# Kernel optimization log

Measured on AMD Instinct MI355X. Metric: run time of the kernel, lower is better.

Reference implementation:

```python
import jax, jax.numpy as jnp
import numpy as np

NUM_LAYERS = 2
NUM_DIR = 2
HID = 512
INP = 1024  # = NUM_DIR * HID so all layers share weight shapes
R = 8
ALPHA = 16
SCALING = ALPHA / R  # 2.0
BATCH = 32
SEQ = 512


def _lstm_dir(x, w_ih, w_hh, b_ih, b_hh, a_ih, bl_ih, a_hh, bl_hh, reverse):
    """One direction of one layer. x: (B,T,D). Returns (out (B,T,H), h_T, c_T)."""
    Bn = x.shape[0]
    # Input-dependent part of the gates is time-parallel: frozen ih matmul,
    # both biases, and the ih LoRA branch (shared A, per-gate B blocks are
    # just the stacked (4H, r) matrix).
    gx = jnp.einsum('btd,gd->btg', x, w_ih) + b_ih + b_hh
    gx = gx + SCALING * jnp.einsum('btr,gr->btg', jnp.einsum('btd,rd->btr', x, a_ih), bl_ih)
    gx = jnp.swapaxes(gx, 0, 1)  # (T,B,4H)
    h0 = jnp.zeros((Bn, HID), x.dtype)
    c0 = jnp.zeros((Bn, HID), x.dtype)

    def step(carry, g_t):
        h, c = carry
        gates = g_t + h @ w_hh.T + SCALING * ((h @ a_hh.T) @ bl_hh.T)
        i, f, g, o = jnp.split(gates, 4, axis=-1)  # torch gate order i,f,g,o
        c = jax.nn.sigmoid(f) * c + jax.nn.sigmoid(i) * jnp.tanh(g)
        h = jax.nn.sigmoid(o) * jnp.tanh(c)
        return (h, c), h

    (hT, cT), hs = jax.lax.scan(step, (h0, c0), gx, reverse=reverse)
    return jnp.swapaxes(hs, 0, 1), hT, cT


def _forward(x, w_ih, w_hh, b_ih, b_hh, a_ih, bl_ih, a_hh, bl_hh):
    layer_in = x
    h_all, c_all = [], []
    for layer in range(NUM_LAYERS):
        outs = []
        for d in range(NUM_DIR):
            idx = layer * NUM_DIR + d
            o, hT, cT = _lstm_dir(layer_in, w_ih[idx], w_hh[idx], b_ih[idx], b_hh[idx],
                                  a_ih[idx], bl_ih[idx], a_hh[idx], bl_hh[idx],
                                  reverse=(d == 1))
            outs.append(o)
            h_all.append(hT)
            c_all.append(cT)
        layer_in = jnp.concatenate(outs, axis=-1)  # (B,T,2H)
        # inter-layer dropout is 0.0 -> identity
    return layer_in, jnp.stack(h_all), jnp.stack(c_all)


def setup_inputs() -> dict:
    key = jax.random.key(0)
    ks = jax.random.split(key, 10)
    G = 4 * HID
    NC = NUM_LAYERS * NUM_DIR  # 4 cells
    s_ih = 1.0 / np.sqrt(INP)
    s_hh = 1.0 / np.sqrt(HID)
    return {
        'x': jax.random.normal(ks[0], (BATCH, SEQ, INP), jnp.float32),
        'w_ih': jax.random.normal(ks[1], (NC, G, INP), jnp.float32) * s_ih,
        'w_hh': jax.random.normal(ks[2], (NC, G, HID), jnp.float32) * s_hh,
        'b_ih': jax.random.normal(ks[3], (NC, G), jnp.float32) * s_hh,
        'b_hh': jax.random.normal(ks[4], (NC, G), jnp.float32) * s_hh,
        'a_ih': jax.random.normal(ks[5], (NC, R, INP), jnp.float32) * s_ih,
        'bl_ih': jax.random.normal(ks[6], (NC, G, R), jnp.float32) * 0.01,
        'a_hh': jax.random.normal(ks[7], (NC, R, HID), jnp.float32) * s_hh,
        'bl_hh': jax.random.normal(ks[8], (NC, G, R), jnp.float32) * 0.01,
    }


def reference(x, w_ih, w_hh, b_ih, b_hh, a_ih, bl_ih, a_hh, bl_hh):
    out, h_n, c_n = _forward(x, w_ih, w_hh, b_ih, b_hh, a_ih, bl_ih, a_hh, bl_hh)
    return out, h_n, c_n
```

## Files before the change

kernel.cpp:

```cpp
#include <hip/hip_runtime.h>
#include <stdint.h>


typedef unsigned short u16;
typedef unsigned long long u64;
typedef __bf16 bf16x8 __attribute__((ext_vector_type(8)));
typedef float f32x4 __attribute__((ext_vector_type(4)));

#define NCELL 4
#define HID 512
#define INP 1024
#define G4 2048
#define BATCH 32
#define SEQ 512
#define RLORA 8
#define NW 16
#define HPW 32
#define HTAGN 8192

__device__ __forceinline__ float bf2f(u16 u) {
  union { uint32_t i; float f; } v;
  v.i = ((uint32_t)u) << 16;
  return v.f;
}
__device__ __forceinline__ u16 f2bf(float f) {
  union { float f; uint32_t i; } v;
  v.f = f;
  uint32_t lsb = (v.i >> 16) & 1;
  return (u16)((v.i + 0x7fffu + lsb) >> 16);
}
__device__ __forceinline__ float sigm(float x) {
  return __builtin_amdgcn_rcpf(1.f + __expf(-x));
}
__device__ __forceinline__ float ftanh(float x) {
  return 1.f - 2.f * __builtin_amdgcn_rcpf(__expf(2.f * x) + 1.f);
}

template <int K>
__global__ void fold_kernel(const float* __restrict__ w, const float* __restrict__ a,
                            const float* __restrict__ bl, u16* __restrict__ weff) {
  int64_t idx = (int64_t)blockIdx.x * blockDim.x + threadIdx.x;
  if (idx >= (int64_t)NCELL * G4 * K) return;
  int d = (int)(idx % K);
  int64_t gc = idx / K;
  int cell = (int)(gc / G4);
  float acc = w[idx];
#pragma unroll
  for (int r = 0; r < RLORA; ++r)
    acc += 2.0f * bl[gc * RLORA + r] * a[(int64_t)cell * RLORA * K + r * K + d];
  weff[idx] = f2bf(acc);
}

__global__ void bias_kernel(const float* __restrict__ b_ih, const float* __restrict__ b_hh,
                            float* __restrict__ bias) {
  int i = blockIdx.x * blockDim.x + threadIdx.x;
  if (i < NCELL * G4) bias[i] = b_ih[i] + b_hh[i];
}

template <bool AF32>
__global__ __launch_bounds__(256) void gemm_kernel(const void* __restrict__ Ain,
                                                   const u16* __restrict__ W,
                                                   const float* __restrict__ bias,
                                                   u16* __restrict__ gx, int tw0, int tw1,
                                                   int CL) {
  __shared__ alignas(16) u16 As[128][72];
  __shared__ alignas(16) u16 Bs[128][72];
  const int tid = threadIdx.x;
  const int dir = blockIdx.z;
  const int m0 = blockIdx.x * 128;
  const int n0 = blockIdx.y * 128;
  const int tw = dir ? tw1 : tw0;
  const int Mc = BATCH * CL;
  const u16* Wc = W + (int64_t)dir * G4 * INP;
  const float* bc = bias + dir * G4;
  u16* gxc = gx + (int64_t)dir * Mc * G4;
  const int wave = tid >> 6, lane = tid & 63;
  const int wm = wave & 1, wn = wave >> 1;
  const int llo = lane & 15, lhi = lane >> 4;

  int64_t aoff[4];
  const u16* bptr[4];
  int srow[4], ssc[4];
#pragma unroll
  for (int i = 0; i < 4; ++i) {
    int s = i * 256 + tid;
    srow[i] = s >> 3;
    ssc[i] = s & 7;
    int lr = m0 + srow[i];
    int b = lr / CL;
    int tt = tw + (lr - b * CL);
    aoff[i] = ((int64_t)b * SEQ + tt) * INP + ssc[i] * 8;
    bptr[i] = Wc + (int64_t)(n0 + srow[i]) * INP + ssc[i] * 8;
  }

  const f32x4 fzero = {0.f, 0.f, 0.f, 0.f};
  f32x4 acc[4][4];
#pragma unroll
  for (int i = 0; i < 4; ++i)
#pragma unroll
    for (int j = 0; j < 4; ++j) acc[i][j] = fzero;

  for (int kt = 0; kt < INP / 64; ++kt) {
    const int kb = kt * 64;
    __syncthreads();
#pragma unroll
    for (int i = 0; i < 4; ++i) {
      if (AF32) {
        const float* src = (const float*)Ain + aoff[i] + kb;
        uint32_t p[4];
#pragma unroll
        for (int q = 0; q < 4; ++q)
          p[q] = (uint32_t)f2bf(src[2 * q]) | ((uint32_t)f2bf(src[2 * q + 1]) << 16);
        *(uint4*)&As[srow[i]][ssc[i] * 8] = make_uint4(p[0], p[1], p[2], p[3]);
      } else {
        *(uint4*)&As[srow[i]][ssc[i] * 8] = *(const uint4*)((const u16*)Ain + aoff[i] + kb);
      }
      *(uint4*)&Bs[srow[i]][ssc[i] * 8] = *(const uint4*)(bptr[i] + kb);
    }
    __syncthreads();
#pragma unroll
    for (int ks = 0; ks < 2; ++ks) {
      bf16x8 af[4], bfr[4];
#pragma unroll
      for (int i = 0; i < 4; ++i) {
        af[i] = *(const bf16x8*)&As[wm * 64 + i * 16 + llo][ks * 32 + lhi * 8];
        bfr[i] = *(const bf16x8*)&Bs[wn * 64 + i * 16 + llo][ks * 32 + lhi * 8];
      }
#pragma unroll
      for (int i = 0; i < 4; ++i)
#pragma unroll
        for (int j = 0; j < 4; ++j)
          acc[i][j] = __builtin_amdgcn_mfma_f32_16x16x32_bf16(af[i], bfr[j], acc[i][j], 0, 0, 0);
    }
  }
#pragma unroll
  for (int i = 0; i < 4; ++i) {
    const int lr0 = m0 + wm * 64 + i * 16 + lhi * 4;
#pragma unroll
    for (int j = 0; j < 4; ++j) {
      const int ncol = n0 + wn * 64 + j * 16 + llo;
      const float bv = bc[ncol];
#pragma unroll
      for (int r = 0; r < 4; ++r) gxc[(int64_t)(lr0 + r) * G4 + ncol] = f2bf(acc[i][j][r] + bv);
    }
  }
}

template <bool OUTF32>
__global__ __launch_bounds__(256, 1) void rec_kernel(
    const u16* __restrict__ gx,
    const u16* __restrict__ Whh,
    u64* __restrict__ htag,
    void* __restrict__ outp,
    float* __restrict__ hn, float* __restrict__ cn,
    float* __restrict__ cstate,
    int cell_base, int s0, int CL) {
  const int tid = threadIdx.x;
  const int dir = blockIdx.x / NW;
  const int wg = blockIdx.x % NW;
  const int hb = wg * HPW;
  const int wave = tid >> 6, lane = tid & 63;
  const int llo = lane & 15, lhi = lane >> 4;
  const int Mc = BATCH * CL;

  const u16* gxc = gx + (int64_t)dir * Mc * G4;
  const u16* Wc = Whh + (int64_t)dir * G4 * HID;
  u64* ht_dir = htag + (int64_t)dir * (2 * HTAGN);
  float* cst = cstate + (int64_t)(cell_base + dir) * BATCH * HID;

  __shared__ alignas(16) u16 h_lds[2 * 16 * 64 * 8];
  __shared__ float g_lds[4][BATCH][HPW + 1];

  uint4 wfrag[2][16];
#pragma unroll
  for (int j = 0; j < 2; ++j)
#pragma unroll
    for (int ks = 0; ks < 16; ++ks) {
      const int col = wave * HID + hb + j * 16 + llo;
      wfrag[j][ks] = *(const uint4*)(Wc + (int64_t)col * HID + ks * 32 + lhi * 8);
    }
  if (s0 == 0) {
    for (int i = tid; i < 2 * 16 * 64 * 8 / 2; i += 256) ((uint32_t*)h_lds)[i] = 0;
  }
  const int cb = tid >> 3, j0 = (tid & 7) * 4;
  float creg[4];
#pragma unroll
  for (int u = 0; u < 4; ++u) creg[u] = (s0 == 0) ? 0.f : cst[cb * HID + hb + j0 + u];
  const int wmt = cb >> 4, wllo = cb & 15, wlhi = j0 >> 3, wjof = j0 & 7;
  const int64_t wfragidx = ((int64_t)((wmt * 16 + wg) * 64 + wlhi * 16 + wllo) * 8 + wjof) >> 2;
  u64* const wpkt_base = ht_dir + 2 * wfragidx;

  for (int s = s0; s < s0 + CL; ++s) {
    const int ls = s - s0;
    const int t = dir ? (SEQ - 1 - s) : s;
    const int lcol = dir ? (CL - 1 - ls) : ls;
    f32x4 acc[2][2];
#pragma unroll
    for (int mt = 0; mt < 2; ++mt)
#pragma unroll
      for (int j = 0; j < 2; ++j) {
        const int col = wave * HID + hb + j * 16 + llo;
#pragma unroll
        for (int r = 0; r < 4; ++r) {
          const int b = mt * 16 + lhi * 4 + r;
          acc[mt][j][r] = bf2f(gxc[(int64_t)(b * CL + lcol) * G4 + col]);
        }
      }
    if (s > 0) {
      u64* src = ht_dir + ((s - 1) & 1) * HTAGN;
      const uint32_t want = (uint32_t)s;
      u64 va[16], vb[16];
#pragma unroll
      for (int k = 0; k < 16; ++k) {
        const int idx = tid + k * 256;
        va[k] = __hip_atomic_load(src + 2 * idx, __ATOMIC_RELAXED, __HIP_MEMORY_SCOPE_AGENT);
        vb[k] = __hip_atomic_load(src + 2 * idx + 1, __ATOMIC_RELAXED, __HIP_MEMORY_SCOPE_AGENT);
      }
      for (;;) {
        uint32_t bad = 0;
#pragma unroll
        for (int k = 0; k < 16; ++k) {
          bad |= ((uint32_t)(va[k] >> 32)) ^ want;
          bad |= ((uint32_t)(vb[k] >> 32)) ^ want;
        }
        if (bad == 0) break;
#pragma unroll
        for (int k = 0; k < 16; ++k) {
          const int idx = tid + k * 256;
          if ((uint32_t)(va[k] >> 32) != want)
            va[k] = __hip_atomic_load(src + 2 * idx, __ATOMIC_RELAXED, __HIP_MEMORY_SCOPE_AGENT);
          if ((uint32_t)(vb[k] >> 32) != want)
            vb[k] =
                __hip_atomic_load(src + 2 * idx + 1, __ATOMIC_RELAXED, __HIP_MEMORY_SCOPE_AGENT);
        }
      }
      __syncthreads();
      u64* dst = (u64*)h_lds;
#pragma unroll
      for (int k = 0; k < 16; ++k) {
        const int idx = tid + k * 256;
        dst[idx] = ((u64)(uint32_t)vb[k] << 32) | (uint32_t)va[k];
      }
    }
    __syncthreads();
#pragma unroll
    for (int ks = 0; ks < 16; ++ks) {
      bf16x8 af[2];
#pragma unroll
      for (int mt = 0; mt < 2; ++mt)
        af[mt] = *(const bf16x8*)&h_lds[((mt * 16 + ks) * 64 + lane) * 8];
#pragma unroll
      for (int mt = 0; mt < 2; ++mt)
#pragma unroll
        for (int j = 0; j < 2; ++j)
          acc[mt][j] = __builtin_amdgcn_mfma_f32_16x16x32_bf16(
              af[mt], __builtin_bit_cast(bf16x8, wfrag[j][ks]), acc[mt][j], 0, 0, 0);
    }
#pragma unroll
    for (int mt = 0; mt < 2; ++mt)
#pragma unroll
      for (int j = 0; j < 2; ++j)
#pragma unroll
        for (int r = 0; r < 4; ++r)
          g_lds[wave][mt * 16 + lhi * 4 + r][j * 16 + llo] = acc[mt][j][r];
    __syncthreads();
    float hv[4], cv[4];
    u16 h16[4];
#pragma unroll
    for (int u = 0; u < 4; ++u) {
      const int jj = j0 + u;
      const float gi = g_lds[0][cb][jj], gf = g_lds[1][cb][jj];
      const float gg = g_lds[2][cb][jj], go = g_lds[3][cb][jj];
      float c = creg[u];
      c = sigm(gf) * c + sigm(gi) * ftanh(gg);
      hv[u] = sigm(go) * ftanh(c);
      cv[u] = c;
      creg[u] = c;
      h16[u] = f2bf(hv[u]);
    }
    {
      const u64 tg = ((u64)(uint32_t)(s + 1)) << 32;
      const u64 lo = (u64)((uint32_t)h16[0] | ((uint32_t)h16[1] << 16));
      const u64 hi = (u64)((uint32_t)h16[2] | ((uint32_t)h16[3] << 16));
      u64* hw = wpkt_base + (s & 1) * HTAGN;
      __hip_atomic_store(hw, tg | lo, __ATOMIC_RELAXED, __HIP_MEMORY_SCOPE_AGENT);
      __hip_atomic_store(hw + 1, tg | hi, __ATOMIC_RELAXED, __HIP_MEMORY_SCOPE_AGENT);
    }
    {
      const int64_t obase = ((int64_t)cb * SEQ + t) * (2 * HID) + dir * HID + hb + j0;
      if (OUTF32) {
        *(float4*)((float*)outp + obase) = make_float4(hv[0], hv[1], hv[2], hv[3]);
      } else {
        uint32_t* ow = (uint32_t*)((u16*)outp + obase);
        ow[0] = (uint32_t)h16[0] | ((uint32_t)h16[1] << 16);
        ow[1] = (uint32_t)h16[2] | ((uint32_t)h16[3] << 16);
      }
      if (s == SEQ - 1) {
        const int cg = cell_base + dir;
        const int64_t nbase = ((int64_t)cg * BATCH + cb) * HID + hb + j0;
        *(float4*)(hn + nbase) = make_float4(hv[0], hv[1], hv[2], hv[3]);
        *(float4*)(cn + nbase) = make_float4(cv[0], cv[1], cv[2], cv[3]);
      }
    }
  }
#pragma unroll
  for (int u = 0; u < 4; ++u) cst[cb * HID + hb + j0 + u] = creg[u];
}

extern "C" void kernel_launch(void* const* d_in, const int* in_sizes, int n_in, void* d_out,
                              int out_size, void* d_ws, size_t ws_size, hipStream_t stream) {
  const float* x = (const float*)d_in[0];
  const float* w_ih = (const float*)d_in[1];
  const float* w_hh = (const float*)d_in[2];
  const float* b_ih = (const float*)d_in[3];
  const float* b_hh = (const float*)d_in[4];
  const float* a_ih = (const float*)d_in[5];
  const float* bl_ih = (const float*)d_in[6];
  const float* a_hh = (const float*)d_in[7];
  const float* bl_hh = (const float*)d_in[8];
  float* out = (float*)d_out;

  char* ws = (char*)d_ws;
  const size_t O_WIH = 0;
  const size_t O_WHH = O_WIH + (size_t)NCELL * G4 * INP * 2;
  const size_t O_BIAS = O_WHH + (size_t)NCELL * G4 * HID * 2;
  const size_t O_CST = O_BIAS + (size_t)NCELL * G4 * 4;
  const size_t O_HBUF = O_CST + (size_t)NCELL * BATCH * HID * 4;
  const size_t O_MID = O_HBUF + (size_t)NCELL * 2 * HTAGN * 8;
  const size_t O_GX = O_MID + (size_t)BATCH * SEQ * 2 * HID * 2;
  u16* w_ih_eff = (u16*)(ws + O_WIH);
  u16* w_hh_eff = (u16*)(ws + O_WHH);
  float* bias = (float*)(ws + O_BIAS);
  float* cstate = (float*)(ws + O_CST);
  u64* hbuf = (u64*)(ws + O_HBUF);
  u16* mid = (u16*)(ws + O_MID);
  u16* gxb = (u16*)(ws + O_GX);

  int CL = 128;
  while (CL > 8 && O_GX + (size_t)2 * BATCH * CL * G4 * 2 > ws_size) CL >>= 1;
  const int nch = SEQ / CL;

  (void)hipMemsetAsync(ws + O_HBUF, 0, (size_t)NCELL * 2 * HTAGN * 8, stream);

  {
    int64_t tot = (int64_t)NCELL * G4 * INP;
    fold_kernel<INP><<<(int)((tot + 255) / 256), 256, 0, stream>>>(w_ih, a_ih, bl_ih, w_ih_eff);
  }
  {
    int64_t tot = (int64_t)NCELL * G4 * HID;
    fold_kernel<HID><<<(int)((tot + 255) / 256), 256, 0, stream>>>(w_hh, a_hh, bl_hh, w_hh_eff);
  }
  bias_kernel<<<(NCELL * G4 + 255) / 256, 256, 0, stream>>>(b_ih, b_hh, bias);

  float* hn = out + (size_t)BATCH * SEQ * (2 * HID);
  float* cn = hn + (size_t)NCELL * BATCH * HID;

  dim3 gemm_grid(BATCH * CL / 128, G4 / 128, 2);
  for (int layer = 0; layer < 2; ++layer) {
    const u16* wih = w_ih_eff + (size_t)layer * 2 * G4 * INP;
    const u16* whh = w_hh_eff + (size_t)layer * 2 * G4 * HID;
    const float* bi = bias + (size_t)layer * 2 * G4;
    u64* hbL = hbuf + (size_t)layer * 4 * HTAGN;
    for (int ci = 0; ci < nch; ++ci) {
      const int tw0 = ci * CL;
      const int tw1 = SEQ - (ci + 1) * CL;
      if (layer == 0) {
        gemm_kernel<true><<<gemm_grid, 256, 0, stream>>>(x, wih, bi, gxb, tw0, tw1, CL);
        rec_kernel<false><<<2 * NW, 256, 0, stream>>>(gxb, whh, hbL, mid, hn, cn, cstate,
                                                      0, ci * CL, CL);
      } else {
        gemm_kernel<false><<<gemm_grid, 256, 0, stream>>>(mid, wih, bi, gxb, tw0, tw1, CL);
        rec_kernel<true><<<2 * NW, 256, 0, stream>>>(gxb, whh, hbL, out, hn, cn, cstate,
                                                     2, ci * CL, CL);
      }
    }
  }
}
```

Before: 4.991 ms.

## Co-locate recurrent workgroups per XCD and restructure h exchange and gate layout

The recurrent kernel now launches 256 blocks. Each block reads its XCD id through s_getreg and joins an atomic election, and only the first two groups of 16 blocks that share an XCD go on to run the two directions. The intent is to keep each direction's cross-workgroup h exchange inside one XCD's L2 instead of crossing dies. Polling becomes 16 inline-asm dwordx4 loads with sc0, and after 16 failed rounds it falls back to an sc1 shadow buffer that every store also writes. The GEMM output is relaid in MFMA fragment order so each step's gate preload is four coalesced u64 loads. The scheme depends on undocumented hwreg numbering and scheduling assumptions, adds redundant stores, and wastes most of the launched blocks.

Measured after the change: 6.531 ms. +30.9%, slower.

```diff
diff --git a/kernel.cpp b/kernel.cpp
--- a/kernel.cpp
+++ b/kernel.cpp
@@ -6,6 +6,7 @@
 typedef unsigned long long u64;
 typedef __bf16 bf16x8 __attribute__((ext_vector_type(8)));
 typedef float f32x4 __attribute__((ext_vector_type(4)));
+typedef int i32x4 __attribute__((ext_vector_type(4)));
 
 #define NCELL 4
 #define HID 512
@@ -29,12 +30,45 @@
   uint32_t lsb = (v.i >> 16) & 1;
   return (u16)((v.i + 0x7fffu + lsb) >> 16);
 }
+__device__ __forceinline__ float asf(uint32_t u) {
+  union { uint32_t i; float f; } v;
+  v.i = u;
+  return v.f;
+}
 __device__ __forceinline__ float sigm(float x) {
   return __builtin_amdgcn_rcpf(1.f + __expf(-x));
 }
 __device__ __forceinline__ float ftanh(float x) {
   return 1.f - 2.f * __builtin_amdgcn_rcpf(__expf(2.f * x) + 1.f);
 }
+
+#define POLL16(Q, BASE, CB)                                            \
+  asm volatile(                                                        \
+      "global_load_dwordx4 %[q0], %[b], off " CB "\n\t"                \
+      "global_load_dwordx4 %[q1], %[b], off offset:16 " CB "\n\t"      \
+      "global_load_dwordx4 %[q2], %[b], off offset:32 " CB "\n\t"      \
+      "global_load_dwordx4 %[q3], %[b], off offset:48 " CB "\n\t"      \
+      "global_load_dwordx4 %[q4], %[b], off offset:64 " CB "\n\t"      \
+      "global_load_dwordx4 %[q5], %[b], off offset:80 " CB "\n\t"      \
+      "global_load_dwordx4 %[q6], %[b], off offset:96 " CB "\n\t"      \
+      "global_load_dwordx4 %[q7], %[b], off offset:112 " CB "\n\t"     \
+      "global_load_dwordx4 %[q8], %[b], off offset:128 " CB "\n\t"     \
+      "global_load_dwordx4 %[q9], %[b], off offset:144 " CB "\n\t"     \
+      "global_load_dwordx4 %[q10], %[b], off offset:160 " CB "\n\t"    \
+      "global_load_dwordx4 %[q11], %[b], off offset:176 " CB "\n\t"    \
+      "global_load_dwordx4 %[q12], %[b], off offset:192 " CB "\n\t"    \
+      "global_load_dwordx4 %[q13], %[b], off offset:208 " CB "\n\t"    \
+      "global_load_dwordx4 %[q14], %[b], off offset:224 " CB "\n\t"    \
+      "global_load_dwordx4 %[q15], %[b], off offset:240 " CB "\n\t"    \
+      "s_waitcnt vmcnt(0)"                                             \
+      : [q0] "=v"(Q[0]), [q1] "=v"(Q[1]), [q2] "=v"(Q[2]),             \
+        [q3] "=v"(Q[3]), [q4] "=v"(Q[4]), [q5] "=v"(Q[5]),             \
+        [q6] "=v"(Q[6]), [q7] "=v"(Q[7]), [q8] "=v"(Q[8]),             \
+        [q9] "=v"(Q[9]), [q10] "=v"(Q[10]), [q11] "=v"(Q[11]),         \
+        [q12] "=v"(Q[12]), [q13] "=v"(Q[13]), [q14] "=v"(Q[14]),       \
+        [q15] "=v"(Q[15])                                              \
+      : [b] "v"(BASE)                                                  \
+      : "memory")
 
 template <int K>
 __global__ void fold_kernel(const float* __restrict__ w, const float* __restrict__ a,
@@ -61,19 +95,20 @@
 __global__ __launch_bounds__(256) void gemm_kernel(const void* __restrict__ Ain,
                                                    const u16* __restrict__ W,
                                                    const float* __restrict__ bias,
-                                                   u16* __restrict__ gx, int tw0, int tw1,
-                                                   int CL) {
+                                                   u16* __restrict__ gx,
+                                                   uint32_t* __restrict__ elect, int tw0,
+                                                   int tw1, int CL, int clsh) {
   __shared__ alignas(16) u16 As[128][72];
   __shared__ alignas(16) u16 Bs[128][72];
   const int tid = threadIdx.x;
+  if (blockIdx.x == 0 && blockIdx.y == 0 && blockIdx.z == 0 && tid < 16) elect[tid] = 0;
   const int dir = blockIdx.z;
   const int m0 = blockIdx.x * 128;
   const int n0 = blockIdx.y * 128;
   const int tw = dir ? tw1 : tw0;
-  const int Mc = BATCH * CL;
   const u16* Wc = W + (int64_t)dir * G4 * INP;
   const float* bc = bias + dir * G4;
-  u16* gxc = gx + (int64_t)dir * Mc * G4;
+  u16* gxc = gx + (size_t)dir * CL * 65536;
   const int wave = tid >> 6, lane = tid & 63;
   const int wm = wave & 1, wn = wave >> 1;
   const int llo = lane & 15, lhi = lane >> 4;
@@ -86,9 +121,10 @@
     int s = i * 256 + tid;
     srow[i] = s >> 3;
     ssc[i] = s & 7;
-    int lr = m0 + srow[i];
-    int b = lr / CL;
-    int tt = tw + (lr - b * CL);
+    int rho = m0 + srow[i];
+    int b = ((rho >> (clsh + 2)) << 2) | (rho & 3);
+    int lcol = (rho >> 2) & (CL - 1);
+    int tt = tw + lcol;
     aoff[i] = ((int64_t)b * SEQ + tt) * INP + ssc[i] * 8;
     bptr[i] = Wc + (int64_t)(n0 + srow[i]) * INP + ssc[i] * 8;
   }
@@ -133,15 +169,25 @@
           acc[i][j] = __builtin_amdgcn_mfma_f32_16x16x32_bf16(af[i], bfr[j], acc[i][j], 0, 0, 0);
     }
   }
-#pragma unroll
-  for (int i = 0; i < 4; ++i) {
-    const int lr0 = m0 + wm * 64 + i * 16 + lhi * 4;
-#pragma unroll
-    for (int j = 0; j < 4; ++j) {
-      const int ncol = n0 + wn * 64 + j * 16 + llo;
-      const float bv = bc[ncol];
-#pragma unroll
-      for (int r = 0; r < 4; ++r) gxc[(int64_t)(lr0 + r) * G4 + ncol] = f2bf(acc[i][j][r] + bv);
+  const int bb = ((m0 >> (clsh + 2)) << 2);
+  const int mt_ = bb >> 4;
+  const int lhiR = (bb >> 2) & 3;
+  const int lc0 = (m0 >> 2) & (CL - 1);
+#pragma unroll
+  for (int jg = 0; jg < 4; ++jg) {
+    const int cb0 = n0 + wn * 64 + jg * 16;
+    const int wgp = (cb0 >> 5) & 15;
+    const int jp = (cb0 >> 4) & 1;
+    const int wvp = cb0 >> 9;
+    const float bv = bc[cb0 + llo];
+    const size_t cbase =
+        (size_t)wgp * 4096 + (size_t)wvp * 1024 + mt_ * 512 + jp * 256 + (lhiR * 16 + llo) * 4;
+#pragma unroll
+    for (int i = 0; i < 4; ++i) {
+      const int lcol = lc0 + wm * 16 + i * 4 + lhi;
+      u64 v = (u64)f2bf(acc[i][jg][0] + bv) | ((u64)f2bf(acc[i][jg][1] + bv) << 16) |
+              ((u64)f2bf(acc[i][jg][2] + bv) << 32) | ((u64)f2bf(acc[i][jg][3] + bv) << 48);
+      *(u64*)(gxc + (size_t)lcol * 65536 + cbase) = v;
     }
   }
 }
@@ -150,26 +196,54 @@
 __global__ __launch_bounds__(256, 1) void rec_kernel(
     const u16* __restrict__ gx,
     const u16* __restrict__ Whh,
-    u64* __restrict__ htag,
+    u64* __restrict__ hbuf,
+    u64* __restrict__ hsh,
+    uint32_t* __restrict__ elect,
     void* __restrict__ outp,
     float* __restrict__ hn, float* __restrict__ cn,
     float* __restrict__ cstate,
     int cell_base, int s0, int CL) {
   const int tid = threadIdx.x;
-  const int dir = blockIdx.x / NW;
-  const int wg = blockIdx.x % NW;
+  __shared__ alignas(16) u16 h_lds[2 * 16 * 64 * 8];
+  __shared__ alignas(16) float g_lds[4][BATCH][HPW + 4];
+  __shared__ uint32_t e_sh[2];
+
+  if (tid == 0) {
+    uint32_t xcc;
+    asm volatile("s_getreg_b32 %0, hwreg(20, 0, 32)" : "=s"(xcc));
+    uint32_t xcd = xcc & 7;
+    uint32_t rank = atomicAdd(&elect[xcd], 1u);
+    uint32_t grp = rank >> 4, grank = rank & 15;
+    uint32_t key = (xcd << 16) | (grp + 1);
+    if (grank == 15) {
+      uint32_t pos = atomicAdd(&elect[8], 1u);
+      if (pos < 2)
+        __hip_atomic_store(&elect[9 + pos], key, __ATOMIC_RELAXED, __HIP_MEMORY_SCOPE_AGENT);
+    }
+    uint32_t dirw;
+    for (;;) {
+      uint32_t m0 = __hip_atomic_load(&elect[9], __ATOMIC_RELAXED, __HIP_MEMORY_SCOPE_AGENT);
+      uint32_t m1 = __hip_atomic_load(&elect[10], __ATOMIC_RELAXED, __HIP_MEMORY_SCOPE_AGENT);
+      if (m0 == key) { dirw = 1; break; }
+      if (m1 == key) { dirw = 2; break; }
+      if (m0 && m1) { dirw = 0; break; }
+    }
+    e_sh[0] = dirw;
+    e_sh[1] = grank;
+  }
+  __syncthreads();
+  if (e_sh[0] == 0) return;
+  const int dir = (int)e_sh[0] - 1;
+  const int wg = (int)e_sh[1];
   const int hb = wg * HPW;
   const int wave = tid >> 6, lane = tid & 63;
   const int llo = lane & 15, lhi = lane >> 4;
-  const int Mc = BATCH * CL;
-
-  const u16* gxc = gx + (int64_t)dir * Mc * G4;
+
+  const u16* gxc = gx + (size_t)dir * CL * 65536;
   const u16* Wc = Whh + (int64_t)dir * G4 * HID;
-  u64* ht_dir = htag + (int64_t)dir * (2 * HTAGN);
+  u64* ht_dir = hbuf + (size_t)dir * (2 * HTAGN);
+  u64* hs_dir = hsh + (size_t)dir * (2 * HTAGN);
   float* cst = cstate + (int64_t)(cell_base + dir) * BATCH * HID;
-
-  __shared__ alignas(16) u16 h_lds[2 * 16 * 64 * 8];
-  __shared__ float g_lds[4][BATCH][HPW + 1];
 
   uint4 wfrag[2][16];
 #pragma unroll
@@ -186,63 +260,61 @@
   float creg[4];
 #pragma unroll
   for (int u = 0; u < 4; ++u) creg[u] = (s0 == 0) ? 0.f : cst[cb * HID + hb + j0 + u];
-  const int wmt = cb >> 4, wllo = cb & 15, wlhi = j0 >> 3, wjof = j0 & 7;
-  const int64_t wfragidx = ((int64_t)((wmt * 16 + wg) * 64 + wlhi * 16 + wllo) * 8 + wjof) >> 2;
-  u64* const wpkt_base = ht_dir + 2 * wfragidx;
+  const int wmt = cb >> 4;
+  const int Fw = ((wmt * 16 + wg) * 64 + (j0 >> 3) * 16 + (cb & 15)) * 2 + ((j0 >> 2) & 1);
+  const int widx = (Fw & 255) * 32 + (Fw >> 8) * 2;
+  int sticky = 0;
 
   for (int s = s0; s < s0 + CL; ++s) {
     const int ls = s - s0;
     const int t = dir ? (SEQ - 1 - s) : s;
     const int lcol = dir ? (CL - 1 - ls) : ls;
+    const u64* gp = (const u64*)gxc + (size_t)lcol * 16384 + wg * 1024 + wave * 256 + lane;
+    u64 g4[4];
+    g4[0] = gp[0];
+    g4[1] = gp[64];
+    g4[2] = gp[128];
+    g4[3] = gp[192];
+    if (s > 0) {
+      const uint32_t want = (uint32_t)s;
+      const int par = (s - 1) & 1;
+      const u64 pb = (u64)(ht_dir + (size_t)par * HTAGN + tid * 32);
+      const u64 pbs = (u64)(hs_dir + (size_t)par * HTAGN + tid * 32);
+      i32x4 q[16];
+      int rounds = 0;
+      for (;;) {
+        if (sticky == 0) {
+          POLL16(q, pb, "sc0");
+        } else {
+          POLL16(q, pbs, "sc0 sc1");
+        }
+        uint32_t bad = 0;
+#pragma unroll
+        for (int k = 0; k < 16; ++k)
+          bad |= ((uint32_t)q[k][1] ^ want) | ((uint32_t)q[k][3] ^ want);
+        if (bad == 0) break;
+        if (++rounds >= 16) sticky = 1;
+      }
+      uint32_t* hd = (uint32_t*)h_lds;
+#pragma unroll
+      for (int k = 0; k < 16; ++k) {
+        hd[2 * tid + k * 512] = (uint32_t)q[k][0];
+        hd[2 * tid + k * 512 + 1] = (uint32_t)q[k][2];
+      }
+    }
+    __syncthreads();
     f32x4 acc[2][2];
 #pragma unroll
     for (int mt = 0; mt < 2; ++mt)
 #pragma unroll
       for (int j = 0; j < 2; ++j) {
-        const int col = wave * HID + hb + j * 16 + llo;
-#pragma unroll
-        for (int r = 0; r < 4; ++r) {
-          const int b = mt * 16 + lhi * 4 + r;
-          acc[mt][j][r] = bf2f(gxc[(int64_t)(b * CL + lcol) * G4 + col]);
-        }
-      }
-    if (s > 0) {
-      u64* src = ht_dir + ((s - 1) & 1) * HTAGN;
-      const uint32_t want = (uint32_t)s;
-      u64 va[16], vb[16];
-#pragma unroll
-      for (int k = 0; k < 16; ++k) {
-        const int idx = tid + k * 256;
-        va[k] = __hip_atomic_load(src + 2 * idx, __ATOMIC_RELAXED, __HIP_MEMORY_SCOPE_AGENT);
-        vb[k] = __hip_atomic_load(src + 2 * idx + 1, __ATOMIC_RELAXED, __HIP_MEMORY_SCOPE_AGENT);
-      }
-      for (;;) {
-        uint32_t bad = 0;
-#pragma unroll
-        for (int k = 0; k < 16; ++k) {
-          bad |= ((uint32_t)(va[k] >> 32)) ^ want;
-          bad |= ((uint32_t)(vb[k] >> 32)) ^ want;
-        }
-        if (bad == 0) break;
-#pragma unroll
-        for (int k = 0; k < 16; ++k) {
-          const int idx = tid + k * 256;
-          if ((uint32_t)(va[k] >> 32) != want)
-            va[k] = __hip_atomic_load(src + 2 * idx, __ATOMIC_RELAXED, __HIP_MEMORY_SCOPE_AGENT);
-          if ((uint32_t)(vb[k] >> 32) != want)
-            vb[k] =
-                __hip_atomic_load(src + 2 * idx + 1, __ATOMIC_RELAXED, __HIP_MEMORY_SCOPE_AGENT);
-        }
-      }
-      __syncthreads();
-      u64* dst = (u64*)h_lds;
-#pragma unroll
-      for (int k = 0; k < 16; ++k) {
-        const int idx = tid + k * 256;
-        dst[idx] = ((u64)(uint32_t)vb[k] << 32) | (uint32_t)va[k];
-      }
-    }
-    __syncthreads();
+        const u64 g = g4[mt * 2 + j];
+        const uint32_t lo = (uint32_t)g, hi = (uint32_t)(g >> 32);
+        acc[mt][j][0] = asf(lo << 16);
+        acc[mt][j][1] = asf(lo & 0xffff0000u);
+        acc[mt][j][2] = asf(hi << 16);
+        acc[mt][j][3] = asf(hi & 0xffff0000u);
+      }
 #pragma unroll
     for (int ks = 0; ks < 16; ++ks) {
       bf16x8 af[2];
@@ -266,25 +338,34 @@
     __syncthreads();
     float hv[4], cv[4];
     u16 h16[4];
-#pragma unroll
-    for (int u = 0; u < 4; ++u) {
-      const int jj = j0 + u;
-      const float gi = g_lds[0][cb][jj], gf = g_lds[1][cb][jj];
-      const float gg = g_lds[2][cb][jj], go = g_lds[3][cb][jj];
-      float c = creg[u];
-      c = sigm(gf) * c + sigm(gi) * ftanh(gg);
-      hv[u] = sigm(go) * ftanh(c);
-      cv[u] = c;
-      creg[u] = c;
-      h16[u] = f2bf(hv[u]);
+    {
+      const f32x4 gi = *(const f32x4*)&g_lds[0][cb][j0];
+      const f32x4 gf = *(const f32x4*)&g_lds[1][cb][j0];
+      const f32x4 gg = *(const f32x4*)&g_lds[2][cb][j0];
+      const f32x4 go = *(const f32x4*)&g_lds[3][cb][j0];
+#pragma unroll
+      for (int u = 0; u < 4; ++u) {
+        float c = creg[u];
+        c = sigm(gf[u]) * c + sigm(gi[u]) * ftanh(gg[u]);
+        hv[u] = sigm(go[u]) * ftanh(c);
+        cv[u] = c;
+        creg[u] = c;
+        h16[u] = f2bf(hv[u]);
+      }
     }
     {
       const u64 tg = ((u64)(uint32_t)(s + 1)) << 32;
-      const u64 lo = (u64)((uint32_t)h16[0] | ((uint32_t)h16[1] << 16));
-      const u64 hi = (u64)((uint32_t)h16[2] | ((uint32_t)h16[3] << 16));
-      u64* hw = wpkt_base + (s & 1) * HTAGN;
-      __hip_atomic_store(hw, tg | lo, __ATOMIC_RELAXED, __HIP_MEMORY_SCOPE_AGENT);
-      __hip_atomic_store(hw + 1, tg | hi, __ATOMIC_RELAXED, __HIP_MEMORY_SCOPE_AGENT);
+      const u64 p0 = tg | (u64)((uint32_t)h16[0] | ((uint32_t)h16[1] << 16));
+      const u64 p1 = tg | (u64)((uint32_t)h16[2] | ((uint32_t)h16[3] << 16));
+      const u64 wa = (u64)(ht_dir + (size_t)(s & 1) * HTAGN + widx);
+      const u64 was = (u64)(hs_dir + (size_t)(s & 1) * HTAGN + widx);
+      asm volatile(
+          "global_store_dwordx2 %[a], %[p0], off sc0\n\t"
+          "global_store_dwordx2 %[a], %[p1], off offset:8 sc0\n\t"
+          "global_store_dwordx2 %[as], %[p0], off sc1\n\t"
+          "global_store_dwordx2 %[as], %[p1], off offset:8 sc1"
+          :: [a] "v"(wa), [as] "v"(was), [p0] "v"(p0), [p1] "v"(p1)
+          : "memory");
     }
     {
       const int64_t obase = ((int64_t)cb * SEQ + t) * (2 * HID) + dir * HID + hb + j0;
@@ -326,21 +407,26 @@
   const size_t O_BIAS = O_WHH + (size_t)NCELL * G4 * HID * 2;
   const size_t O_CST = O_BIAS + (size_t)NCELL * G4 * 4;
   const size_t O_HBUF = O_CST + (size_t)NCELL * BATCH * HID * 4;
-  const size_t O_MID = O_HBUF + (size_t)NCELL * 2 * HTAGN * 8;
+  const size_t O_HSH = O_HBUF + (size_t)2 * 2 * 2 * HTAGN * 8;
+  const size_t O_ELECT = O_HSH + (size_t)2 * 2 * 2 * HTAGN * 8;
+  const size_t O_MID = O_ELECT + 256;
   const size_t O_GX = O_MID + (size_t)BATCH * SEQ * 2 * HID * 2;
   u16* w_ih_eff = (u16*)(ws + O_WIH);
   u16* w_hh_eff = (u16*)(ws + O_WHH);
   float* bias = (float*)(ws + O_BIAS);
   float* cstate = (float*)(ws + O_CST);
   u64* hbuf = (u64*)(ws + O_HBUF);
+  u64* hshadow = (u64*)(ws + O_HSH);
+  uint32_t* elect = (uint32_t*)(ws + O_ELECT);
   u16* mid = (u16*)(ws + O_MID);
   u16* gxb = (u16*)(ws + O_GX);
 
   int CL = 128;
-  while (CL > 8 && O_GX + (size_t)2 * BATCH * CL * G4 * 2 > ws_size) CL >>= 1;
+  while (CL > 32 && O_GX + (size_t)2 * BATCH * CL * G4 * 2 > ws_size) CL >>= 1;
   const int nch = SEQ / CL;
-
-  (void)hipMemsetAsync(ws + O_HBUF, 0, (size_t)NCELL * 2 * HTAGN * 8, stream);
+  int clsh = 31 - __builtin_clz((unsigned)CL);
+
+  (void)hipMemsetAsync(ws + O_HBUF, 0, (size_t)2 * 2 * 2 * 2 * HTAGN * 8, stream);
 
   {
     int64_t tot = (int64_t)NCELL * G4 * INP;
@@ -361,18 +447,21 @@
     const u16* whh = w_hh_eff + (size_t)layer * 2 * G4 * HID;
     const float* bi = bias + (size_t)layer * 2 * G4;
     u64* hbL = hbuf + (size_t)layer * 4 * HTAGN;
+    u64* hsL = hshadow + (size_t)layer * 4 * HTAGN;
     for (int ci = 0; ci < nch; ++ci) {
       const int tw0 = ci * CL;
       const int tw1 = SEQ - (ci + 1) * CL;
       if (layer == 0) {
-        gemm_kernel<true><<<gemm_grid, 256, 0, stream>>>(x, wih, bi, gxb, tw0, tw1, CL);
-        rec_kernel<false><<<2 * NW, 256, 0, stream>>>(gxb, whh, hbL, mid, hn, cn, cstate,
-                                                      0, ci * CL, CL);
+        gemm_kernel<true><<<gemm_grid, 256, 0, stream>>>(x, wih, bi, gxb, elect, tw0, tw1, CL,
+                                                         clsh);
+        rec_kernel<false><<<256, 256, 0, stream>>>(gxb, whh, hbL, hsL, elect, mid, hn, cn,
+                                                   cstate, 0, ci * CL, CL);
       } else {
-        gemm_kernel<false><<<gemm_grid, 256, 0, stream>>>(mid, wih, bi, gxb, tw0, tw1, CL);
-        rec_kernel<true><<<2 * NW, 256, 0, stream>>>(gxb, whh, hbL, out, hn, cn, cstate,
-                                                     2, ci * CL, CL);
-      }
-    }
-  }
-}
+        gemm_kernel<false><<<gemm_grid, 256, 0, stream>>>(mid, wih, bi, gxb, elect, tw0, tw1,
+                                                          CL, clsh);
+        rec_kernel<true><<<256, 256, 0, stream>>>(gxb, whh, hbL, hsL, elect, out, hn, cn,
+                                                  cstate, 2, ci * CL, CL);
+      }
+    }
+  }
+}
```
